# Kernel tuning notes

Measured on AMD Instinct MI355X. Metric: run time of the kernel, lower is better.

The kernel has to match this reference:

```python
import jax, jax.numpy as jnp
import numpy as np

N_USERS = 100000
N_ITEMS = 200000
N_NODES = N_USERS + N_ITEMS
NNZ = 9600000
EMBED_DIM = 64
N_LAYERS = 3


def setup_inputs() -> dict:
    key = jax.random.key(0)
    k1, k2, k3, k4, k5 = jax.random.split(key, 5)
    edge_rows = jax.random.randint(k1, (NNZ,), 0, N_NODES, dtype=jnp.int32)
    edge_cols = jax.random.randint(k2, (NNZ,), 0, N_NODES, dtype=jnp.int32)
    # normalized adjacency values are small positive floats
    edge_vals = jax.random.uniform(k3, (NNZ,), dtype=jnp.float32) * 0.05
    user_emb = jax.random.normal(k4, (N_USERS, EMBED_DIM), dtype=jnp.float32) * 0.1
    item_emb = jax.random.normal(k5, (N_ITEMS, EMBED_DIM), dtype=jnp.float32) * 0.1
    return {
        "edge_rows": edge_rows,
        "edge_cols": edge_cols,
        "edge_vals": edge_vals,
        "user_emb": user_emb,
        "item_emb": item_emb,
        "n_users": N_USERS,
    }


def _spmm(rows, cols, vals, x, n):
    # y = A @ x where A is COO sparse [n, n]
    msgs = vals[:, None] * x[cols]            # [nnz, d]
    return jax.ops.segment_sum(msgs, rows, num_segments=n)


def reference(edge_rows, edge_cols, edge_vals, user_emb, item_emb, n_users):
    all_emb = jnp.concatenate([user_emb, item_emb], axis=0)  # [N, d]
    n = all_emb.shape[0]
    acc = all_emb
    emb = all_emb
    for _ in range(N_LAYERS):
        emb = _spmm(edge_rows, edge_cols, edge_vals, emb, n)
        acc = acc + emb
    final = acc / jnp.asarray(N_LAYERS + 1, dtype=all_emb.dtype)
    user_final = final[:n_users]
    item_final = final[n_users:]
    return user_final, item_final
```

## Files before the change

### kernel.cpp

```cpp
#include <hip/hip_runtime.h>


constexpr int N_USERS_C = 100000;
constexpr int N_NODES_C = 300000;
constexpr int NNZ_C     = 9600000;
constexpr int DIM       = 64;
constexpr int TOT4      = N_NODES_C * DIM / 4;
constexpr int USER4     = N_USERS_C * DIM / 4;

constexpr int BKT_SHIFT = 7;
constexpr int BKT_ROWS  = 128;
constexpr int NBKT      = (N_NODES_C + BKT_ROWS - 1) / BKT_ROWS;
constexpr int CPAD      = 16;
constexpr int COL_MASK  = (1 << 19) - 1;

__device__ inline unsigned pack_bf16(float a, float b) {
    unsigned ua = __float_as_uint(a);
    unsigned ub = __float_as_uint(b);
    ua += 0x7fffu + ((ua >> 16) & 1u);
    ub += 0x7fffu + ((ub >> 16) & 1u);
    return (ua >> 16) | (ub & 0xffff0000u);
}
__device__ inline float bf_lo(unsigned w) { return __uint_as_float(w << 16); }
__device__ inline float bf_hi(unsigned w) { return __uint_as_float(w & 0xffff0000u); }


__global__ void __launch_bounds__(256) init_concat_bf16(
    const float4* __restrict__ user4,
    const float4* __restrict__ item4,
    float4* __restrict__ acc4,
    uint2*  __restrict__ xb)
{
    int i = blockIdx.x * 256 + threadIdx.x;
    if (i >= TOT4) return;
    float4 v = (i < USER4) ? user4[i] : item4[i - USER4];
    acc4[i] = v;
    xb[i] = make_uint2(pack_bf16(v.x, v.y), pack_bf16(v.z, v.w));
}


__global__ void __launch_bounds__(1024) bucket_hist_lds(
    const int* __restrict__ rows, int* __restrict__ countsP)
{
    __shared__ int h[NBKT];
    for (int i = threadIdx.x; i < NBKT; i += 1024) h[i] = 0;
    __syncthreads();
    int per = (NNZ_C + gridDim.x - 1) / gridDim.x;
    int s = blockIdx.x * per;
    int e = min(s + per, NNZ_C);
    for (int i = s + (int)threadIdx.x; i < e; i += 1024)
        atomicAdd(&h[rows[i] >> BKT_SHIFT], 1);
    __syncthreads();
    for (int i = threadIdx.x; i < NBKT; i += 1024) {
        int c = h[i];
        if (c) atomicAdd(&countsP[i * CPAD], c);
    }
}

__global__ void __launch_bounds__(1024) bucket_scan(
    const int* __restrict__ countsP,
    int* __restrict__ bstart,
    int* __restrict__ cursorP)
{
    __shared__ int lds[1024];
    int t = threadIdx.x;
    int base = t * 3;
    int v[3]; int s = 0;
    #pragma unroll
    for (int j = 0; j < 3; ++j) {
        int idx = base + j;
        v[j] = (idx < NBKT) ? countsP[idx * CPAD] : 0;
        s += v[j];
    }
    lds[t] = s;
    __syncthreads();
    for (int off = 1; off < 1024; off <<= 1) {
        int x = (t >= off) ? lds[t - off] : 0;
        __syncthreads();
        lds[t] += x;
        __syncthreads();
    }
    int run = (t == 0) ? 0 : lds[t - 1];
    #pragma unroll
    for (int j = 0; j < 3; ++j) {
        int idx = base + j;
        if (idx < NBKT) {
            bstart[idx] = run;
            cursorP[idx * CPAD] = run;
        }
        run += v[j];
    }
    if (t == 1023) bstart[NBKT] = lds[1023];
}

constexpr int STAGE_T   = 12288;
constexpr int STAGE_EPT = STAGE_T / 1024;

__global__ void __launch_bounds__(1024) bin_stage(
    const int* __restrict__ rows, const int* __restrict__ cols,
    const float* __restrict__ vals, int* __restrict__ cursorP,
    int2* __restrict__ binned)
{
    __shared__ int2 stage[STAGE_T];
    __shared__ unsigned short destB[STAGE_T];
    __shared__ int hist[NBKT];
    __shared__ int basep[NBKT];
    __shared__ int part[16];

    int t  = threadIdx.x;
    int e0 = blockIdx.x * STAGE_T;
    int cnt = min(STAGE_T, NNZ_C - e0);

    for (int i = t; i < NBKT; i += 1024) hist[i] = 0;
    __syncthreads();

    int  myB[STAGE_EPT];
    int  myR[STAGE_EPT];
    int2 myP[STAGE_EPT];
    #pragma unroll
    for (int j = 0; j < STAGE_EPT; ++j) {
        int i = t + j * 1024;
        myB[j] = -1;
        if (i < cnt) {
            int r = rows[e0 + i];
            int b = r >> BKT_SHIFT;
            myB[j] = b;
            myP[j] = make_int2(((r & (BKT_ROWS - 1)) << 19) | cols[e0 + i],
                               __float_as_int(vals[e0 + i]));
            myR[j] = atomicAdd(&hist[b], 1);
        }
    }
    __syncthreads();

    int idx0 = t * 3;
    int v0 = (idx0     < NBKT) ? hist[idx0]     : 0;
    int v1 = (idx0 + 1 < NBKT) ? hist[idx0 + 1] : 0;
    int v2 = (idx0 + 2 < NBKT) ? hist[idx0 + 2] : 0;
    int s  = v0 + v1 + v2;

    int lane = t & 63, wid = t >> 6;
    int x = s;
    #pragma unroll
    for (int d = 1; d < 64; d <<= 1) {
        int y = __shfl_up(x, d);
        if (lane >= d) x += y;
    }
    if (lane == 63) part[wid] = x;
    __syncthreads();
    if (wid == 0 && lane < 16) {
        int w = part[lane];
        #pragma unroll
        for (int d = 1; d < 16; d <<= 1) {
            int y = __shfl_up(w, d);
            if (lane >= d) w += y;
        }
        part[lane] = w;
    }
    __syncthreads();
    int excl = ((wid == 0) ? 0 : part[wid - 1]) + (x - s);
    if (idx0     < NBKT) basep[idx0]     = excl;          excl += v0;
    if (idx0 + 1 < NBKT) basep[idx0 + 1] = excl;          excl += v1;
    if (idx0 + 2 < NBKT) basep[idx0 + 2] = excl;
    __syncthreads();

    for (int i = t; i < NBKT; i += 1024) {
        int c = hist[i];
        hist[i] = (c > 0) ? (atomicAdd(&cursorP[i * CPAD], c) - basep[i]) : 0;
    }
    #pragma unroll
    for (int j = 0; j < STAGE_EPT; ++j) {
        if (myB[j] >= 0) {
            int q = basep[myB[j]] + myR[j];
            stage[q] = myP[j];
            destB[q] = (unsigned short)myB[j];
        }
    }
    __syncthreads();

    #pragma unroll
    for (int j = 0; j < STAGE_EPT; ++j) {
        int p = t + j * 1024;
        if (p < cnt) {
            int b = destB[p];
            binned[hist[b] + p] = stage[p];
        }
    }
}

__global__ void __launch_bounds__(256) sort_bucket(
    const int2* __restrict__ binned,
    const int*  __restrict__ bstart,
    int2* __restrict__ binned2,
    int*  __restrict__ rowStart)
{
    __shared__ int hist[BKT_ROWS];
    __shared__ int scanb[BKT_ROWS];
    __shared__ int cur[BKT_ROWS];

    int b = blockIdx.x;
    int t = threadIdx.x;
    int s = bstart[b];
    int n = bstart[b + 1] - s;

    if (t < BKT_ROWS) hist[t] = 0;
    __syncthreads();

    for (int i = t; i < n; i += 256)
        atomicAdd(&hist[binned[s + i].x >> 19], 1);
    __syncthreads();

    if (t < BKT_ROWS) scanb[t] = hist[t];
    __syncthreads();
    for (int off = 1; off < BKT_ROWS; off <<= 1) {
        int v = (t < BKT_ROWS && t >= off) ? scanb[t - off] : 0;
        __syncthreads();
        if (t < BKT_ROWS) scanb[t] += v;
        __syncthreads();
    }

    int rowBase = b << BKT_SHIFT;
    int nRows = min(BKT_ROWS, N_NODES_C - rowBase);
    if (t < BKT_ROWS) {
        int st = (t == 0) ? 0 : scanb[t - 1];
        cur[t] = st;
        if (t < nRows) rowStart[rowBase + t] = s + st;
    }
    if (b == 0 && t == 0) rowStart[N_NODES_C] = NNZ_C;
    __syncthreads();

    for (int i = t; i < n; i += 256) {
        int2 p = binned[s + i];
        int rl = p.x >> 19;
        int pos = atomicAdd(&cur[rl], 1);
        binned2[s + pos] = make_int2(p.x & COL_MASK, p.y);
    }
}

__global__ void __launch_bounds__(256) spmm_pull_bf16(
    const int2* __restrict__ edges,
    const int*  __restrict__ rowStart,
    const uint4* __restrict__ xb,
    uint4* __restrict__ xb_next,
    float4* __restrict__ acc,
    float scale)
{
    int tid = blockIdx.x * 256 + threadIdx.x;
    int row = tid >> 3;
    if (row >= N_NODES_C) return;
    int q = tid & 7;

    int s = rowStart[row];
    int e = rowStart[row + 1];

    float y0 = 0.f, y1 = 0.f, y2 = 0.f, y3 = 0.f;
    float y4 = 0.f, y5 = 0.f, y6 = 0.f, y7 = 0.f;

    int i = s;
    for (; i + 1 < e; i += 2) {
        int2 pa = edges[i];
        int2 pb = edges[i + 1];
        uint4 ua = xb[(size_t)pa.x * 8 + q];
        uint4 ub = xb[(size_t)pb.x * 8 + q];
        float va = __int_as_float(pa.y);
        float vb = __int_as_float(pb.y);
        y0 += va * bf_lo(ua.x); y1 += va * bf_hi(ua.x);
        y2 += va * bf_lo(ua.y); y3 += va * bf_hi(ua.y);
        y4 += va * bf_lo(ua.z); y5 += va * bf_hi(ua.z);
        y6 += va * bf_lo(ua.w); y7 += va * bf_hi(ua.w);
        y0 += vb * bf_lo(ub.x); y1 += vb * bf_hi(ub.x);
        y2 += vb * bf_lo(ub.y); y3 += vb * bf_hi(ub.y);
        y4 += vb * bf_lo(ub.z); y5 += vb * bf_hi(ub.z);
        y6 += vb * bf_lo(ub.w); y7 += vb * bf_hi(ub.w);
    }
    if (i < e) {
        int2 p = edges[i];
        uint4 u = xb[(size_t)p.x * 8 + q];
        float v = __int_as_float(p.y);
        y0 += v * bf_lo(u.x); y1 += v * bf_hi(u.x);
        y2 += v * bf_lo(u.y); y3 += v * bf_hi(u.y);
        y4 += v * bf_lo(u.z); y5 += v * bf_hi(u.z);
        y6 += v * bf_lo(u.w); y7 += v * bf_hi(u.w);
    }

    uint4 o;
    o.x = pack_bf16(y0, y1);
    o.y = pack_bf16(y2, y3);
    o.z = pack_bf16(y4, y5);
    o.w = pack_bf16(y6, y7);
    xb_next[(size_t)row * 8 + q] = o;

    size_t base = (size_t)row * 16 + q * 2;
    float4 a0 = acc[base];
    float4 a1 = acc[base + 1];
    a0.x = (a0.x + y0) * scale;
    a0.y = (a0.y + y1) * scale;
    a0.z = (a0.z + y2) * scale;
    a0.w = (a0.w + y3) * scale;
    a1.x = (a1.x + y4) * scale;
    a1.y = (a1.y + y5) * scale;
    a1.z = (a1.z + y6) * scale;
    a1.w = (a1.w + y7) * scale;
    acc[base]     = a0;
    acc[base + 1] = a1;
}


__global__ void __launch_bounds__(256) init_concat_f32(
    const float4* __restrict__ user4,
    const float4* __restrict__ item4,
    float4* __restrict__ emb4,
    float4* __restrict__ acc4)
{
    int i = blockIdx.x * 256 + threadIdx.x;
    if (i >= TOT4) return;
    float4 v = (i < USER4) ? user4[i] : item4[i - USER4];
    emb4[i] = v;
    acc4[i] = v;
}

__global__ void __launch_bounds__(256) spmm_scatter(
    const int*   __restrict__ rows,
    const int*   __restrict__ cols,
    const float* __restrict__ vals,
    const float* __restrict__ x,
    float*       __restrict__ y)
{
    long long tid = (long long)blockIdx.x * 256 + threadIdx.x;
    int e = (int)(tid >> 4);
    if (e >= NNZ_C) return;
    int q = (int)(tid & 15);
    int   r = rows[e];
    int   c = cols[e];
    float v = vals[e];
    float4 xv = ((const float4*)x)[c * 16 + q];
    float* yp = y + (long long)r * DIM + q * 4;
    atomicAdd(yp + 0, v * xv.x);
    atomicAdd(yp + 1, v * xv.y);
    atomicAdd(yp + 2, v * xv.z);
    atomicAdd(yp + 3, v * xv.w);
}

__global__ void __launch_bounds__(256) acc_add(
    const float4* __restrict__ nxt, float4* __restrict__ acc, float scale)
{
    int i = blockIdx.x * 256 + threadIdx.x;
    if (i >= TOT4) return;
    float4 a = acc[i];
    float4 n = nxt[i];
    a.x = (a.x + n.x) * scale;
    a.y = (a.y + n.y) * scale;
    a.z = (a.z + n.z) * scale;
    a.w = (a.w + n.w) * scale;
    acc[i] = a;
}


extern "C" void kernel_launch(void* const* d_in, const int* in_sizes, int n_in,
                              void* d_out, int out_size, void* d_ws, size_t ws_size,
                              hipStream_t stream)
{
    const int*   rows = (const int*)  d_in[0];
    const int*   cols = (const int*)  d_in[1];
    const float* vals = (const float*)d_in[2];
    const float* uemb = (const float*)d_in[3];
    const float* iemb = (const float*)d_in[4];
    float*       out  = (float*)d_out;

    const size_t embBytes   = (size_t)N_NODES_C * DIM * sizeof(float);
    const size_t bfBytes    = (size_t)N_NODES_C * DIM * 2;
    const size_t edgeBytes  = (size_t)NNZ_C * sizeof(int2);
    const size_t padBytes   = (size_t)NBKT * CPAD * sizeof(int);
    const size_t rsBytes    = (size_t)(N_NODES_C + 1) * sizeof(int);

    char* w = (char*)d_ws;
    size_t off = 0;
    unsigned* xbf0   = (unsigned*)(w + off); off += bfBytes;
    unsigned* xbf1   = (unsigned*)(w + off); off += bfBytes;
    int2*  binned    = (int2*) (w + off); off += edgeBytes;
    int2*  binned2   = (int2*) (w + off); off += edgeBytes;
    int*   rowStart  = (int*)  (w + off); off += rsBytes;
    int*   countsP   = (int*)  (w + off); off += padBytes;
    int*   cursorP   = (int*)  (w + off); off += padBytes;
    int*   bstart    = (int*)  (w + off); off += (size_t)(NBKT + 1) * sizeof(int) + 4096;
    const size_t needed = off;

    const int gridE    = (TOT4 + 255) / 256;
    const int gridPull = (N_NODES_C * 8) / 256;
    const int gridBin  = (NNZ_C + STAGE_T - 1) / STAGE_T;

    if (ws_size >= needed) {
        init_concat_bf16<<<gridE, 256, 0, stream>>>(
            (const float4*)uemb, (const float4*)iemb, (float4*)out, (uint2*)xbf0);

        hipMemsetAsync(countsP, 0, padBytes, stream);
        bucket_hist_lds<<<256, 1024, 0, stream>>>(rows, countsP);
        bucket_scan<<<1, 1024, 0, stream>>>(countsP, bstart, cursorP);
        bin_stage<<<gridBin, 1024, 0, stream>>>(rows, cols, vals, cursorP, binned);
        sort_bucket<<<NBKT, 256, 0, stream>>>(binned, bstart, binned2, rowStart);

        unsigned* cur = xbf0;
        unsigned* nxt = xbf1;
        for (int layer = 0; layer < 3; ++layer) {
            float scale = (layer == 2) ? 0.25f : 1.0f;
            spmm_pull_bf16<<<gridPull, 256, 0, stream>>>(
                binned2, rowStart, (const uint4*)cur, (uint4*)nxt,
                (float4*)out, scale);
            unsigned* t = cur; cur = nxt; nxt = t;
        }
    } else {
        float* buf0 = (float*)d_ws;
        float* buf1 = (float*)((char*)d_ws + embBytes);
        init_concat_f32<<<gridE, 256, 0, stream>>>(
            (const float4*)uemb, (const float4*)iemb, (float4*)buf0, (float4*)out);
        const long long sThreads = (long long)NNZ_C * 16;
        const int gridS = (int)((sThreads + 255) / 256);
        float* cur = buf0;
        float* nxt = buf1;
        for (int layer = 0; layer < 3; ++layer) {
            hipMemsetAsync(nxt, 0, embBytes, stream);
            spmm_scatter<<<gridS, 256, 0, stream>>>(rows, cols, vals, cur, nxt);
            float scale = (layer == 2) ? 0.25f : 1.0f;
            acc_add<<<gridE, 256, 0, stream>>>((const float4*)nxt, (float4*)out, scale);
            float* t = cur; cur = nxt; nxt = t;
        }
    }
}
```

Before: 1.096 ms.

## Sort edges by column within rows, fold acc init into first layer, halve bin stage

sort_bucket now stages each bucket in LDS and rank-sorts every row's edges by column index, so the gather in the SpMM reads neighbour embeddings in ascending order. The goal is better cache locality during the three gather-heavy layers. The float accumulator is no longer written by the init kernel; the first SpMM layer reads the original user and item embeddings directly, saving one full write and read of the fp32 buffer. The bin_stage tile is halved and sort_bucket moves to 512 threads; the per-row O(n^2) rank sort adds preprocessing cost.

```diff
diff --git a/kernel.cpp b/kernel.cpp
--- a/kernel.cpp
+++ b/kernel.cpp
@@ -28,13 +28,11 @@
 __global__ void __launch_bounds__(256) init_concat_bf16(
     const float4* __restrict__ user4,
     const float4* __restrict__ item4,
-    float4* __restrict__ acc4,
     uint2*  __restrict__ xb)
 {
     int i = blockIdx.x * 256 + threadIdx.x;
     if (i >= TOT4) return;
     float4 v = (i < USER4) ? user4[i] : item4[i - USER4];
-    acc4[i] = v;
     xb[i] = make_uint2(pack_bf16(v.x, v.y), pack_bf16(v.z, v.w));
 }
 
@@ -93,7 +91,7 @@
     if (t == 1023) bstart[NBKT] = lds[1023];
 }
 
-constexpr int STAGE_T   = 12288;
+constexpr int STAGE_T   = 6144;
 constexpr int STAGE_EPT = STAGE_T / 1024;
 
 __global__ void __launch_bounds__(1024) bin_stage(
@@ -187,7 +185,9 @@
     }
 }
 
-__global__ void __launch_bounds__(256) sort_bucket(
+constexpr int SB_CAP = 4608;
+
+__global__ void __launch_bounds__(512) sort_bucket(
     const int2* __restrict__ binned,
     const int*  __restrict__ bstart,
     int2* __restrict__ binned2,
@@ -196,6 +196,7 @@
     __shared__ int hist[BKT_ROWS];
     __shared__ int scanb[BKT_ROWS];
     __shared__ int cur[BKT_ROWS];
+    __shared__ int2 stage[SB_CAP];
 
     int b = blockIdx.x;
     int t = threadIdx.x;
@@ -205,7 +206,7 @@
     if (t < BKT_ROWS) hist[t] = 0;
     __syncthreads();
 
-    for (int i = t; i < n; i += 256)
+    for (int i = t; i < n; i += 512)
         atomicAdd(&hist[binned[s + i].x >> 19], 1);
     __syncthreads();
 
@@ -228,11 +229,46 @@
     if (b == 0 && t == 0) rowStart[N_NODES_C] = NNZ_C;
     __syncthreads();
 
-    for (int i = t; i < n; i += 256) {
-        int2 p = binned[s + i];
-        int rl = p.x >> 19;
-        int pos = atomicAdd(&cur[rl], 1);
-        binned2[s + pos] = make_int2(p.x & COL_MASK, p.y);
+    if (n <= SB_CAP) {
+        for (int i = t; i < n; i += 512) {
+            int2 p = binned[s + i];
+            int rl = p.x >> 19;
+            int pos = atomicAdd(&cur[rl], 1);
+            if (pos < SB_CAP) stage[pos] = p;
+        }
+        __syncthreads();
+        int lane = t & 63, wid = t >> 6;
+        for (int r = wid * 16; r < wid * 16 + 16; ++r) {
+            int st = (r == 0) ? 0 : scanb[r - 1];
+            int nr = scanb[r] - st;
+            if (nr <= 0) continue;
+            if (nr <= 128) {
+                int i0 = lane, i1 = lane + 64;
+                int2 e0 = make_int2(0, 0), e1 = make_int2(0, 0);
+                if (i0 < nr) e0 = stage[st + i0];
+                if (i1 < nr) e1 = stage[st + i1];
+                int r0 = 0, r1 = 0;
+                for (int j = 0; j < nr; ++j) {
+                    int kj = stage[st + j].x;
+                    r0 += (i0 < nr) && ((kj < e0.x) || (kj == e0.x && j < i0));
+                    r1 += (i1 < nr) && ((kj < e1.x) || (kj == e1.x && j < i1));
+                }
+                if (i0 < nr && r0 < nr) binned2[s + st + r0] = make_int2(e0.x & COL_MASK, e0.y);
+                if (i1 < nr && r1 < nr) binned2[s + st + r1] = make_int2(e1.x & COL_MASK, e1.y);
+            } else {
+                for (int i = lane; i < nr; i += 64) {
+                    int2 p = stage[st + i];
+                    binned2[s + st + i] = make_int2(p.x & COL_MASK, p.y);
+                }
+            }
+        }
+    } else {
+        for (int i = t; i < n; i += 512) {
+            int2 p = binned[s + i];
+            int rl = p.x >> 19;
+            int pos = atomicAdd(&cur[rl], 1);
+            binned2[s + pos] = make_int2(p.x & COL_MASK, p.y);
+        }
     }
 }
 
@@ -242,6 +278,9 @@
     const uint4* __restrict__ xb,
     uint4* __restrict__ xb_next,
     float4* __restrict__ acc,
+    const float4* __restrict__ x0u,
+    const float4* __restrict__ x0i,
+    int layer0,
     float scale)
 {
     int tid = blockIdx.x * 256 + threadIdx.x;
@@ -290,8 +329,17 @@
     xb_next[(size_t)row * 8 + q] = o;
 
     size_t base = (size_t)row * 16 + q * 2;
-    float4 a0 = acc[base];
-    float4 a1 = acc[base + 1];
+    float4 a0, a1;
+    if (layer0) {
+        const float4* src = (row < N_USERS_C)
+            ? x0u + (size_t)row * 16 + q * 2
+            : x0i + (size_t)(row - N_USERS_C) * 16 + q * 2;
+        a0 = src[0];
+        a1 = src[1];
+    } else {
+        a0 = acc[base];
+        a1 = acc[base + 1];
+    }
     a0.x = (a0.x + y0) * scale;
     a0.y = (a0.y + y1) * scale;
     a0.z = (a0.z + y2) * scale;
@@ -390,13 +438,13 @@
 
     if (ws_size >= needed) {
         init_concat_bf16<<<gridE, 256, 0, stream>>>(
-            (const float4*)uemb, (const float4*)iemb, (float4*)out, (uint2*)xbf0);
+            (const float4*)uemb, (const float4*)iemb, (uint2*)xbf0);
 
         hipMemsetAsync(countsP, 0, padBytes, stream);
         bucket_hist_lds<<<256, 1024, 0, stream>>>(rows, countsP);
         bucket_scan<<<1, 1024, 0, stream>>>(countsP, bstart, cursorP);
         bin_stage<<<gridBin, 1024, 0, stream>>>(rows, cols, vals, cursorP, binned);
-        sort_bucket<<<NBKT, 256, 0, stream>>>(binned, bstart, binned2, rowStart);
+        sort_bucket<<<NBKT, 512, 0, stream>>>(binned, bstart, binned2, rowStart);
 
         unsigned* cur = xbf0;
         unsigned* nxt = xbf1;
@@ -404,7 +452,8 @@
             float scale = (layer == 2) ? 0.25f : 1.0f;
             spmm_pull_bf16<<<gridPull, 256, 0, stream>>>(
                 binned2, rowStart, (const uint4*)cur, (uint4*)nxt,
-                (float4*)out, scale);
+                (float4*)out, (const float4*)uemb, (const float4*)iemb,
+                (layer == 0) ? 1 : 0, scale);
             unsigned* t = cur; cur = nxt; nxt = t;
         }
     } else {
```

Measured after the change: 1.235 ms. +12.6%, slower.

## Enlarge row buckets to 512, shrink bin staging, fold acc init into first SpMM layer

Applied to the files above, without the earlier changes.

Bucket width grows from 128 to 512 rows, so there are far fewer buckets (586). The scans now use one bucket per thread, bin_stage uses smaller per-block staging tiles, and sort_bucket runs with 1024 threads per bucket. The fp32 accumulator is no longer written in the init kernel. Instead, the first SpMM layer reads the original user and item embeddings directly as its accumulator base, which removes one full fp32 write and read pass over the embeddings. The tradeoffs are larger per-bucket sort work and more bin_stage blocks, each with more atomics against the global cursor.

```diff
diff --git a/kernel.cpp b/kernel.cpp
--- a/kernel.cpp
+++ b/kernel.cpp
@@ -8,8 +8,8 @@
 constexpr int TOT4      = N_NODES_C * DIM / 4;
 constexpr int USER4     = N_USERS_C * DIM / 4;
 
-constexpr int BKT_SHIFT = 7;
-constexpr int BKT_ROWS  = 128;
+constexpr int BKT_SHIFT = 9;
+constexpr int BKT_ROWS  = 512;
 constexpr int NBKT      = (N_NODES_C + BKT_ROWS - 1) / BKT_ROWS;
 constexpr int CPAD      = 16;
 constexpr int COL_MASK  = (1 << 19) - 1;
@@ -28,13 +28,11 @@
 __global__ void __launch_bounds__(256) init_concat_bf16(
     const float4* __restrict__ user4,
     const float4* __restrict__ item4,
-    float4* __restrict__ acc4,
     uint2*  __restrict__ xb)
 {
     int i = blockIdx.x * 256 + threadIdx.x;
     if (i >= TOT4) return;
     float4 v = (i < USER4) ? user4[i] : item4[i - USER4];
-    acc4[i] = v;
     xb[i] = make_uint2(pack_bf16(v.x, v.y), pack_bf16(v.z, v.w));
 }
 
@@ -64,15 +62,8 @@
 {
     __shared__ int lds[1024];
     int t = threadIdx.x;
-    int base = t * 3;
-    int v[3]; int s = 0;
-    #pragma unroll
-    for (int j = 0; j < 3; ++j) {
-        int idx = base + j;
-        v[j] = (idx < NBKT) ? countsP[idx * CPAD] : 0;
-        s += v[j];
-    }
-    lds[t] = s;
+    int v = (t < NBKT) ? countsP[t * CPAD] : 0;
+    lds[t] = v;
     __syncthreads();
     for (int off = 1; off < 1024; off <<= 1) {
         int x = (t >= off) ? lds[t - off] : 0;
@@ -80,20 +71,15 @@
         lds[t] += x;
         __syncthreads();
     }
-    int run = (t == 0) ? 0 : lds[t - 1];
-    #pragma unroll
-    for (int j = 0; j < 3; ++j) {
-        int idx = base + j;
-        if (idx < NBKT) {
-            bstart[idx] = run;
-            cursorP[idx * CPAD] = run;
-        }
-        run += v[j];
+    int excl = lds[t] - v;
+    if (t < NBKT) {
+        bstart[t] = excl;
+        cursorP[t * CPAD] = excl;
     }
     if (t == 1023) bstart[NBKT] = lds[1023];
 }
 
-constexpr int STAGE_T   = 12288;
+constexpr int STAGE_T   = 6144;
 constexpr int STAGE_EPT = STAGE_T / 1024;
 
 __global__ void __launch_bounds__(1024) bin_stage(
@@ -132,14 +118,10 @@
     }
     __syncthreads();
 
-    int idx0 = t * 3;
-    int v0 = (idx0     < NBKT) ? hist[idx0]     : 0;
-    int v1 = (idx0 + 1 < NBKT) ? hist[idx0 + 1] : 0;
-    int v2 = (idx0 + 2 < NBKT) ? hist[idx0 + 2] : 0;
-    int s  = v0 + v1 + v2;
+    int v0 = (t < NBKT) ? hist[t] : 0;
 
     int lane = t & 63, wid = t >> 6;
-    int x = s;
+    int x = v0;
     #pragma unroll
     for (int d = 1; d < 64; d <<= 1) {
         int y = __shfl_up(x, d);
@@ -157,10 +139,8 @@
         part[lane] = w;
     }
     __syncthreads();
-    int excl = ((wid == 0) ? 0 : part[wid - 1]) + (x - s);
-    if (idx0     < NBKT) basep[idx0]     = excl;          excl += v0;
-    if (idx0 + 1 < NBKT) basep[idx0 + 1] = excl;          excl += v1;
-    if (idx0 + 2 < NBKT) basep[idx0 + 2] = excl;
+    int excl = ((wid == 0) ? 0 : part[wid - 1]) + (x - v0);
+    if (t < NBKT) basep[t] = excl;
     __syncthreads();
 
     for (int i = t; i < NBKT; i += 1024) {
@@ -187,7 +167,7 @@
     }
 }
 
-__global__ void __launch_bounds__(256) sort_bucket(
+__global__ void __launch_bounds__(1024) sort_bucket(
     const int2* __restrict__ binned,
     const int*  __restrict__ bstart,
     int2* __restrict__ binned2,
@@ -205,7 +185,7 @@
     if (t < BKT_ROWS) hist[t] = 0;
     __syncthreads();
 
-    for (int i = t; i < n; i += 256)
+    for (int i = t; i < n; i += 1024)
         atomicAdd(&hist[binned[s + i].x >> 19], 1);
     __syncthreads();
 
@@ -228,7 +208,7 @@
     if (b == 0 && t == 0) rowStart[N_NODES_C] = NNZ_C;
     __syncthreads();
 
-    for (int i = t; i < n; i += 256) {
+    for (int i = t; i < n; i += 1024) {
         int2 p = binned[s + i];
         int rl = p.x >> 19;
         int pos = atomicAdd(&cur[rl], 1);
@@ -242,6 +222,9 @@
     const uint4* __restrict__ xb,
     uint4* __restrict__ xb_next,
     float4* __restrict__ acc,
+    const float4* __restrict__ x0u,
+    const float4* __restrict__ x0i,
+    int layer0,
     float scale)
 {
     int tid = blockIdx.x * 256 + threadIdx.x;
@@ -290,8 +273,17 @@
     xb_next[(size_t)row * 8 + q] = o;
 
     size_t base = (size_t)row * 16 + q * 2;
-    float4 a0 = acc[base];
-    float4 a1 = acc[base + 1];
+    float4 a0, a1;
+    if (layer0) {
+        const float4* src = (row < N_USERS_C)
+            ? x0u + (size_t)row * 16 + q * 2
+            : x0i + (size_t)(row - N_USERS_C) * 16 + q * 2;
+        a0 = src[0];
+        a1 = src[1];
+    } else {
+        a0 = acc[base];
+        a1 = acc[base + 1];
+    }
     a0.x = (a0.x + y0) * scale;
     a0.y = (a0.y + y1) * scale;
     a0.z = (a0.z + y2) * scale;
@@ -390,13 +382,13 @@
 
     if (ws_size >= needed) {
         init_concat_bf16<<<gridE, 256, 0, stream>>>(
-            (const float4*)uemb, (const float4*)iemb, (float4*)out, (uint2*)xbf0);
+            (const float4*)uemb, (const float4*)iemb, (uint2*)xbf0);
 
         hipMemsetAsync(countsP, 0, padBytes, stream);
         bucket_hist_lds<<<256, 1024, 0, stream>>>(rows, countsP);
         bucket_scan<<<1, 1024, 0, stream>>>(countsP, bstart, cursorP);
         bin_stage<<<gridBin, 1024, 0, stream>>>(rows, cols, vals, cursorP, binned);
-        sort_bucket<<<NBKT, 256, 0, stream>>>(binned, bstart, binned2, rowStart);
+        sort_bucket<<<NBKT, 1024, 0, stream>>>(binned, bstart, binned2, rowStart);
 
         unsigned* cur = xbf0;
         unsigned* nxt = xbf1;
@@ -404,7 +396,8 @@
             float scale = (layer == 2) ? 0.25f : 1.0f;
             spmm_pull_bf16<<<gridPull, 256, 0, stream>>>(
                 binned2, rowStart, (const uint4*)cur, (uint4*)nxt,
-                (float4*)out, scale);
+                (float4*)out, (const float4*)uemb, (const float4*)iemb,
+                (layer == 0) ? 1 : 0, scale);
             unsigned* t = cur; cur = nxt; nxt = t;
         }
     } else {
```

Measured after the change: 1.038 ms. 5.3% less time.
